# Kernel tuning notes

Measured on AMD Instinct MI355X. Metric: run time of the kernel, lower is better.

The kernel has to match this reference:

```python
import jax, jax.numpy as jnp
import numpy as np

IMAGE_SIZE = 512.0
CENTER_VARIANCE = 0.1
SIZE_VARIANCE = 0.2
NMS_THRESHOLD = 0.45
MAX_CANDIDATES = 400
MAX_PER_IMAGE = 100


def setup_inputs() -> dict:
    key = jax.random.key(0)
    k1, k2, k3, k4 = jax.random.split(key, 4)
    B, P, C = 16, 32768, 81
    cls_logits = jax.random.normal(k1, (B, P, C), dtype=jnp.float32)
    bbox_pred = jax.random.normal(k2, (B, P, 4), dtype=jnp.float32)
    # priors in center form [cx, cy, w, h], normalized coords
    centers = jax.random.uniform(k3, (P, 2), dtype=jnp.float32)
    sizes = jax.random.uniform(k4, (P, 2), dtype=jnp.float32, minval=0.02, maxval=0.4)
    priors = jnp.concatenate([centers, sizes], axis=-1)
    return {"cls_logits": cls_logits, "bbox_pred": bbox_pred, "priors": priors}


def _decode_boxes(locations, priors):
    # locations_to_boxes + center_to_corner_form
    cxy = locations[..., :2] * CENTER_VARIANCE * priors[..., 2:] + priors[..., :2]
    wh = jnp.exp(locations[..., 2:] * SIZE_VARIANCE) * priors[..., 2:]
    return jnp.concatenate([cxy - wh * 0.5, cxy + wh * 0.5], axis=-1)  # [P, 4] xyxy


def _pairwise_iou(boxes):
    # boxes: [N, 4] xyxy
    lt = jnp.maximum(boxes[:, None, :2], boxes[None, :, :2])
    rb = jnp.minimum(boxes[:, None, 2:], boxes[None, :, 2:])
    wh = jnp.clip(rb - lt, 0.0)
    inter = wh[..., 0] * wh[..., 1]
    area = (boxes[:, 2] - boxes[:, 0]) * (boxes[:, 3] - boxes[:, 1])
    union = area[:, None] + area[None, :] - inter
    return inter / jnp.maximum(union, 1e-12)


def _batched_nms_keep(boxes, scores, labels, iou_threshold):
    # boxes sorted by descending score; class-offset trick then greedy NMS
    max_coord = jnp.max(boxes)
    offset = labels.astype(boxes.dtype) * (max_coord + 1.0)
    ious = _pairwise_iou(boxes + offset[:, None])  # [N, N]
    n = boxes.shape[0]
    order = jnp.arange(n)

    def body(i, keep):
        suppress = keep[i] & (ious[i] > iou_threshold) & (order > i)
        return keep & ~suppress

    return jax.lax.fori_loop(0, n, body, jnp.ones((n,), dtype=bool))


def _per_image(logits, locations, priors):
    # logits: [P, C], locations: [P, 4], priors: [P, 4]
    num_classes = logits.shape[-1]
    cm1 = num_classes - 1  # foreground classes (background col 0 dropped)
    scores_all = jax.nn.log_softmax(logits, axis=-1)[:, 1:].reshape(-1)  # [P*(C-1)]
    boxes = _decode_boxes(locations, priors)  # [P, 4]
    # sort_keep_top_k: argsort descending, take top max_candidates
    top_scores, flat_idx = jax.lax.top_k(scores_all, MAX_CANDIDATES)
    box_idx = flat_idx // cm1
    labels = flat_idx % cm1 + 1
    top_boxes = boxes[box_idx] * IMAGE_SIZE  # width == height == image_size
    keep = _batched_nms_keep(top_boxes, top_scores, labels, NMS_THRESHOLD)
    # torch keep[:max_per_image]: first MAX_PER_IMAGE kept entries in score order.
    # Entries are already score-sorted, so top_k on masked scores recovers them.
    masked = jnp.where(keep, top_scores, -jnp.inf)
    _, kidx = jax.lax.top_k(masked, MAX_PER_IMAGE)
    out_scores = jnp.where(keep[kidx], top_scores[kidx], -jnp.inf)  # -inf marks padding
    return top_boxes[kidx], labels[kidx], out_scores


def reference(cls_logits, bbox_pred, priors):
    boxes, labels, scores = jax.vmap(_per_image, in_axes=(0, 0, None))(
        cls_logits, bbox_pred, priors
    )
    return boxes, labels, scores
```

## Files before the change

kernel.cpp:

```cpp
#include <hip/hip_runtime.h>
#include <math.h>

#define BATCH 16
#define P 32768
#define C 81
#define CM1 80
#define NCAND 400
#define NOUT 100
#define NBINS 256
#define SMIN_F (-3.0f)
#define BIN_SCALE (NBINS / 3.0f)
#define SORTN 1024
#define ROWCAP 1024
#define IMG_SZ 512.0f
#define NMS_THR 0.45f
#define NWORDS 7
#define NPAD 448
#define RPB 64

#define OFF_HIST 0
#define OFF_MAXSC 16384
#define NEED_WS (OFF_MAXSC + (size_t)BATCH * P * 4)

__device__ __forceinline__ int score_bin(float sc) {
    int b = (int)((sc - SMIN_F) * BIN_SCALE);
    return b < 0 ? 0 : (b > NBINS - 1 ? NBINS - 1 : b);
}

__device__ __forceinline__ void quad_stats(const float* __restrict__ rowp, int q,
                                           float r[21], float& m, float& l, float& fg) {
#pragma unroll
    for (int k = 0; k < 21; ++k) {
        int c = 4 * k + q;
        r[k] = (c < C) ? rowp[c] : -INFINITY;
    }
    float mm = -INFINITY;
#pragma unroll
    for (int k = 0; k < 21; ++k) mm = fmaxf(mm, r[k]);
    mm = fmaxf(mm, __shfl_xor(mm, 1));
    mm = fmaxf(mm, __shfl_xor(mm, 2));
    float s = 0.0f;
#pragma unroll
    for (int k = 0; k < 21; ++k) {
        int c = 4 * k + q;
        if (c < C) s += __expf(r[k] - mm);
    }
    s += __shfl_xor(s, 1);
    s += __shfl_xor(s, 2);
    float fgm = -INFINITY;
#pragma unroll
    for (int k = 0; k < 21; ++k) {
        int c = 4 * k + q;
        if (c >= 1 && c < C) fgm = fmaxf(fgm, r[k]);
    }
    fgm = fmaxf(fgm, __shfl_xor(fgm, 1));
    fgm = fmaxf(fgm, __shfl_xor(fgm, 2));
    m = mm;
    l = __logf(s);
    fg = fgm;
}

__device__ __forceinline__ unsigned long long pack_key(float v, unsigned id) {
    unsigned bits = __float_as_uint(v);
    unsigned u = (bits & 0x80000000u) ? ~bits : (bits | 0x80000000u);
    return ((unsigned long long)(~u) << 32) | id;
}

__global__ __launch_bounds__(256) void k_hist(const float* __restrict__ logits,
                                              unsigned* __restrict__ hist,
                                              float* __restrict__ maxsc) {
    __shared__ float tile[RPB * C];
    __shared__ unsigned lh[NBINS];
    int img = blockIdx.y;
    int row0 = blockIdx.x * RPB;
    lh[threadIdx.x] = 0;
    const float4* g4 = (const float4*)(logits + ((size_t)img * P + row0) * C);
    float4* t4 = (float4*)tile;
#pragma unroll
    for (int i = 0; i < 6; ++i) {
        int idx = threadIdx.x + i * 256;
        if (idx < RPB * C / 4) t4[idx] = g4[idx];
    }
    __syncthreads();
    int quad = threadIdx.x >> 2, q = threadIdx.x & 3;
    const float* rowp = tile + quad * C;
    float r[21], m, l, fg;
    quad_stats(rowp, q, r, m, l, fg);
    if (q == 0) maxsc[(size_t)img * P + row0 + quad] = (fg - m) - l;
#pragma unroll
    for (int k = 0; k < 21; ++k) {
        int c = 4 * k + q;
        if (c >= 1 && c < C) {
            float sc = (r[k] - m) - l;
            if (sc > SMIN_F) atomicAdd(&lh[score_bin(sc)], 1u);
        }
    }
    __syncthreads();
    unsigned h = lh[threadIdx.x];
    if (h) atomicAdd(&hist[(size_t)img * NBINS + threadIdx.x], h);
}

__global__ __launch_bounds__(1024) void k_post(const float* __restrict__ logits,
                                               const float* __restrict__ bbox,
                                               const float* __restrict__ priors,
                                               const unsigned* __restrict__ hist,
                                               const float* __restrict__ maxsc,
                                               float* __restrict__ out) {
    __shared__ int tb_sh, nrows_sh, ncand_sh;
    __shared__ int rowlist[ROWCAP];
    __shared__ unsigned long long key[SORTN];
    __shared__ float x1[NCAND], y1[NCAND], x2[NCAND], y2[NCAND];
    __shared__ float ox1[NPAD], oy1[NPAD], ox2[NPAD], oy2[NPAD], areas[NPAD];
    __shared__ float scs[NCAND];
    __shared__ int lab[NCAND];
    __shared__ unsigned long long M[NPAD][NWORDS];
    __shared__ unsigned long long keepw_s[NWORDS];
    __shared__ int wpre_s[NWORDS + 1];
    __shared__ float wred[16];
    __shared__ float maxc_sh;
    __shared__ int kidx[NOUT];

    int img = blockIdx.x;
    int tid = threadIdx.x;
    int lane = tid & 63;
    int wv = tid >> 6;

    if (tid == 0) { tb_sh = 0; nrows_sh = 0; ncand_sh = 0; }

    float4 msv[P / 4 / 1024];
    const float4* ms4 = (const float4*)(maxsc + (size_t)img * P);
#pragma unroll
    for (int i = 0; i < P / 4 / 1024; ++i) msv[i] = ms4[tid + i * 1024];

    key[tid] = pack_key(-INFINITY, 0x7FFFFFFFu);

    if (wv == 0) {
        uint4 h4 = ((const uint4*)(hist + (size_t)img * NBINS))[lane];
        unsigned own = h4.x + h4.y + h4.z + h4.w;
        unsigned acc = own;
#pragma unroll
        for (int off = 1; off < 64; off <<= 1) {
            unsigned t = __shfl_down(acc, off);
            if (lane + off < 64) acc += t;
        }
        unsigned above = acc - own;
        unsigned s3 = above + h4.w;
        unsigned s2 = s3 + h4.z;
        unsigned s1 = s2 + h4.y;
        unsigned s0 = s1 + h4.x;
        int best = -1;
        if (s0 >= NCAND) best = 4 * lane + 0;
        if (s1 >= NCAND) best = 4 * lane + 1;
        if (s2 >= NCAND) best = 4 * lane + 2;
        if (s3 >= NCAND) best = 4 * lane + 3;
#pragma unroll
        for (int off = 32; off >= 1; off >>= 1) {
            int o = __shfl_xor(best, off);
            best = best > o ? best : o;
        }
        if (lane == 0) tb_sh = best < 0 ? 0 : best;
    }
    __syncthreads();
    int tb = tb_sh;

#pragma unroll
    for (int i = 0; i < P / 4 / 1024; ++i) {
        float4 v4 = msv[i];
        int rbase = (tid + i * 1024) * 4;
        float vv[4] = {v4.x, v4.y, v4.z, v4.w};
#pragma unroll
        for (int j = 0; j < 4; ++j) {
            if (vv[j] > SMIN_F && score_bin(vv[j]) >= tb) {
                int pos = atomicAdd(&nrows_sh, 1);
                if (pos < ROWCAP) rowlist[pos] = rbase + j;
            }
        }
    }
    __syncthreads();
    int nrows = nrows_sh;
    if (nrows > ROWCAP) nrows = ROWCAP;

    {
        int quad = tid >> 2, q = tid & 3;
        for (int base = 0; base < nrows; base += 256) {
            int ri = base + quad;
            if (ri < nrows) {
                int row = rowlist[ri];
                const float* rowp = logits + ((size_t)img * P + row) * C;
                float r[21], m, l, fg;
                quad_stats(rowp, q, r, m, l, fg);
#pragma unroll
                for (int k = 0; k < 21; ++k) {
                    int c = 4 * k + q;
                    if (c >= 1 && c < C) {
                        float sc = (r[k] - m) - l;
                        if (sc > SMIN_F && score_bin(sc) >= tb) {
                            int pos = atomicAdd(&ncand_sh, 1);
                            if (pos < SORTN)
                                key[pos] = pack_key(sc, (unsigned)(row * CM1 + c - 1));
                        }
                    }
                }
            }
        }
    }
    __syncthreads();

    unsigned long long kr = key[tid];
#pragma unroll
    for (int k2 = 2; k2 <= 64; k2 <<= 1) {
        for (int j = k2 >> 1; j > 0; j >>= 1) {
            unsigned long long pv = __shfl_xor(kr, j);
            bool takeMin = (((tid & j) == 0) == ((tid & k2) == 0));
            bool sel = takeMin ? (pv < kr) : (pv > kr);
            if (sel) kr = pv;
        }
    }
    for (int k2 = 128; k2 <= SORTN; k2 <<= 1) {
        for (int j = k2 >> 1; j >= 64; j >>= 1) {
            __syncthreads();
            key[tid] = kr;
            __syncthreads();
            unsigned long long pv = key[tid ^ j];
            bool takeMin = (((tid & j) == 0) == ((tid & k2) == 0));
            bool sel = takeMin ? (pv < kr) : (pv > kr);
            if (sel) kr = pv;
        }
#pragma unroll
        for (int j = 32; j > 0; j >>= 1) {
            unsigned long long pv = __shfl_xor(kr, j);
            bool takeMin = (((tid & j) == 0) == ((tid & k2) == 0));
            bool sel = takeMin ? (pv < kr) : (pv > kr);
            if (sel) kr = pv;
        }
    }

    if (tid < NCAND) {
        unsigned uu = ~(unsigned)(kr >> 32);
        unsigned bits = (uu & 0x80000000u) ? (uu & 0x7FFFFFFFu) : ~uu;
        scs[tid] = __uint_as_float(bits);
        unsigned f = (unsigned)(kr & 0xFFFFFFFFu);
        if (f > (unsigned)(P * CM1 - 1)) f = (unsigned)(P * CM1 - 1);
        int p = (int)(f / CM1);
        int c = (int)(f % CM1) + 1;
        const float* lp = bbox + ((size_t)img * P + p) * 4;
        const float* pp = priors + (size_t)p * 4;
        float cx = lp[0] * 0.1f * pp[2] + pp[0];
        float cy = lp[1] * 0.1f * pp[3] + pp[1];
        float w = expf(lp[2] * 0.2f) * pp[2];
        float h = expf(lp[3] * 0.2f) * pp[3];
        x1[tid] = (cx - w * 0.5f) * IMG_SZ;
        y1[tid] = (cy - h * 0.5f) * IMG_SZ;
        x2[tid] = (cx + w * 0.5f) * IMG_SZ;
        y2[tid] = (cy + h * 0.5f) * IMG_SZ;
        lab[tid] = c;
    }
    __syncthreads();

    float mx = -INFINITY;
    if (tid < NCAND) mx = fmaxf(fmaxf(x1[tid], y1[tid]), fmaxf(x2[tid], y2[tid]));
#pragma unroll
    for (int off = 32; off >= 1; off >>= 1) mx = fmaxf(mx, __shfl_xor(mx, off));
    if (lane == 0) wred[wv] = mx;
    __syncthreads();
    if (tid == 0) {
        float mm = -INFINITY;
        for (int t = 0; t < 16; ++t) mm = fmaxf(mm, wred[t]);
        maxc_sh = mm;
    }
    __syncthreads();

    if (tid < NPAD) {
        if (tid < NCAND) {
            float off = (float)lab[tid] * (maxc_sh + 1.0f);
            ox1[tid] = x1[tid] + off;
            oy1[tid] = y1[tid] + off;
            ox2[tid] = x2[tid] + off;
            oy2[tid] = y2[tid] + off;
            areas[tid] = (ox2[tid] - ox1[tid]) * (oy2[tid] - oy1[tid]);
        } else {
            ox1[tid] = 1e30f; oy1[tid] = 1e30f;
            ox2[tid] = 1e30f; oy2[tid] = 1e30f;
            areas[tid] = 0.0f;
        }
    }
    __syncthreads();

    for (int i = wv; i < NCAND; i += 16) {
        float a1 = ox1[i], b1 = oy1[i], a2 = ox2[i], b2 = oy2[i], ar = areas[i];
#pragma unroll
        for (int wd = 0; wd < NWORDS; ++wd) {
            int j = wd * 64 + lane;
            float iw_ = fmaxf(fminf(a2, ox2[j]) - fmaxf(a1, ox1[j]), 0.0f);
            float ih_ = fmaxf(fminf(b2, oy2[j]) - fmaxf(b1, oy1[j]), 0.0f);
            float inter = iw_ * ih_;
            float uni = ar + areas[j] - inter;
            float iou = inter / fmaxf(uni, 1e-12f);
            unsigned long long bits = __ballot(iou > NMS_THR);
            if (lane == 0) M[i][wd] = bits;
        }
    }
    __syncthreads();

    if (wv == 0) {
        unsigned long long acc[NWORDS] = {0, 0, 0, 0, 0, 0, 0};
        unsigned long long keepw[NWORDS];
#pragma unroll
        for (int iw = 0; iw < NWORDS; ++iw) {
            unsigned long long mrow[NWORDS];
#pragma unroll
            for (int w = iw; w < NWORDS; ++w) mrow[w] = M[iw * 64 + lane][w];
            unsigned long long sup = acc[iw];
            unsigned long long K = 0;
            int nb = (iw == NWORDS - 1) ? (NCAND - 64 * (NWORDS - 1)) : 64;
            for (int ib = 0; ib < nb; ++ib) {
                if (!((sup >> ib) & 1ull)) {
                    K |= (1ull << ib);
                    int lo, hi;
                    lo = __builtin_amdgcn_readlane((int)(unsigned)mrow[iw], ib);
                    hi = __builtin_amdgcn_readlane((int)(unsigned)(mrow[iw] >> 32), ib);
                    sup |= ((unsigned long long)(unsigned)hi << 32) | (unsigned)lo;
#pragma unroll
                    for (int w = iw + 1; w < NWORDS; ++w) {
                        lo = __builtin_amdgcn_readlane((int)(unsigned)mrow[w], ib);
                        hi = __builtin_amdgcn_readlane((int)(unsigned)(mrow[w] >> 32), ib);
                        acc[w] |= ((unsigned long long)(unsigned)hi << 32) | (unsigned)lo;
                    }
                }
            }
            keepw[iw] = K;
        }
        if (lane == 0) {
            int a = 0;
#pragma unroll
            for (int w = 0; w < NWORDS; ++w) {
                keepw_s[w] = keepw[w];
                wpre_s[w] = a;
                a += __popcll(keepw[w]);
            }
            wpre_s[NWORDS] = a;
        }
    }
    __syncthreads();

    if (tid < NCAND) {
        int w = tid >> 6, bb = tid & 63;
        unsigned long long kwv = keepw_s[w];
        bool kp = (kwv >> bb) & 1ull;
        unsigned long long below_mask = (bb == 0) ? 0ull : (~0ull >> (64 - bb));
        int below = wpre_s[w] + __popcll(kwv & below_mask);
        int nkept = wpre_s[NWORDS];
        int pos = kp ? below : nkept + (tid - below);
        if (pos < NOUT) kidx[pos] = tid;
    }
    __syncthreads();

    if (tid < NOUT) {
        int i = kidx[tid];
        bool kp = (keepw_s[i >> 6] >> (i & 63)) & 1ull;
        float* ob = out + ((size_t)img * NOUT + tid) * 4;
        ob[0] = x1[i];
        ob[1] = y1[i];
        ob[2] = x2[i];
        ob[3] = y2[i];
        out[(size_t)BATCH * NOUT * 4 + (size_t)img * NOUT + tid] = (float)lab[i];
        out[(size_t)BATCH * NOUT * 4 + (size_t)BATCH * NOUT + (size_t)img * NOUT + tid] =
            kp ? scs[i] : -INFINITY;
    }
}

extern "C" void kernel_launch(void* const* d_in, const int* in_sizes, int n_in,
                              void* d_out, int out_size, void* d_ws, size_t ws_size,
                              hipStream_t stream) {
    const float* logits = (const float*)d_in[0];
    const float* bbox = (const float*)d_in[1];
    const float* priors = (const float*)d_in[2];
    float* out = (float*)d_out;
    char* ws = (char*)d_ws;

    unsigned* hist = (unsigned*)(ws + OFF_HIST);
    float* maxsc = (float*)(ws + OFF_MAXSC);

    hipMemsetAsync(ws, 0, OFF_MAXSC, stream);

    dim3 g1(P / RPB, BATCH);
    k_hist<<<g1, 256, 0, stream>>>(logits, hist, maxsc);
    k_post<<<BATCH, 1024, 0, stream>>>(logits, bbox, priors, hist, maxsc, out);
}
```

Baseline: 339.6 us.

## Emit candidate keys from histogram pass instead of recomputing rows in post kernel

```diff
diff --git a/kernel.cpp b/kernel.cpp
--- a/kernel.cpp
+++ b/kernel.cpp
@@ -11,16 +11,18 @@
 #define SMIN_F (-3.0f)
 #define BIN_SCALE (NBINS / 3.0f)
 #define SORTN 1024
-#define ROWCAP 1024
 #define IMG_SZ 512.0f
 #define NMS_THR 0.45f
 #define NWORDS 7
 #define NPAD 448
 #define RPB 64
+#define LCAP 2048
+#define CAND_CAP 131072
 
 #define OFF_HIST 0
-#define OFF_MAXSC 16384
-#define NEED_WS (OFF_MAXSC + (size_t)BATCH * P * 4)
+#define OFF_GCNT 16384
+#define OFF_CAND 16448
+#define NEED_WS (OFF_CAND + (size_t)BATCH * CAND_CAP * 8)
 
 __device__ __forceinline__ int score_bin(float sc) {
     int b = (int)((sc - SMIN_F) * BIN_SCALE);
@@ -66,14 +68,25 @@
     return ((unsigned long long)(~u) << 32) | id;
 }
 
+__device__ __forceinline__ float unpack_score(unsigned long long kk) {
+    unsigned uu = ~(unsigned)(kk >> 32);
+    unsigned bits = (uu & 0x80000000u) ? (uu & 0x7FFFFFFFu) : ~uu;
+    return __uint_as_float(bits);
+}
+
 __global__ __launch_bounds__(256) void k_hist(const float* __restrict__ logits,
                                               unsigned* __restrict__ hist,
-                                              float* __restrict__ maxsc) {
+                                              unsigned* __restrict__ gcnt,
+                                              unsigned long long* __restrict__ cand) {
     __shared__ float tile[RPB * C];
     __shared__ unsigned lh[NBINS];
+    __shared__ unsigned long long lc[LCAP];
+    __shared__ int lcnt_sh;
+    __shared__ int base_sh;
     int img = blockIdx.y;
     int row0 = blockIdx.x * RPB;
     lh[threadIdx.x] = 0;
+    if (threadIdx.x == 0) lcnt_sh = 0;
     const float4* g4 = (const float4*)(logits + ((size_t)img * P + row0) * C);
     float4* t4 = (float4*)tile;
 #pragma unroll
@@ -86,28 +99,42 @@
     const float* rowp = tile + quad * C;
     float r[21], m, l, fg;
     quad_stats(rowp, q, r, m, l, fg);
-    if (q == 0) maxsc[(size_t)img * P + row0 + quad] = (fg - m) - l;
+    (void)fg;
+    int row = row0 + quad;
 #pragma unroll
     for (int k = 0; k < 21; ++k) {
         int c = 4 * k + q;
         if (c >= 1 && c < C) {
             float sc = (r[k] - m) - l;
-            if (sc > SMIN_F) atomicAdd(&lh[score_bin(sc)], 1u);
+            if (sc > SMIN_F) {
+                atomicAdd(&lh[score_bin(sc)], 1u);
+                int pos = atomicAdd(&lcnt_sh, 1);
+                if (pos < LCAP) lc[pos] = pack_key(sc, (unsigned)(row * CM1 + c - 1));
+            }
         }
     }
     __syncthreads();
     unsigned h = lh[threadIdx.x];
     if (h) atomicAdd(&hist[(size_t)img * NBINS + threadIdx.x], h);
-}
-
-__global__ __launch_bounds__(1024) void k_post(const float* __restrict__ logits,
-                                               const float* __restrict__ bbox,
+    int n = lcnt_sh;
+    if (n > LCAP) n = LCAP;
+    if (threadIdx.x == 0) base_sh = (int)atomicAdd(&gcnt[img], (unsigned)n);
+    __syncthreads();
+    int base = base_sh;
+    unsigned long long* dst = cand + (size_t)img * CAND_CAP;
+    for (int i = threadIdx.x; i < n; i += 256) {
+        int pos = base + i;
+        if (pos < CAND_CAP) dst[pos] = lc[i];
+    }
+}
+
+__global__ __launch_bounds__(1024) void k_post(const float* __restrict__ bbox,
                                                const float* __restrict__ priors,
                                                const unsigned* __restrict__ hist,
-                                               const float* __restrict__ maxsc,
+                                               const unsigned* __restrict__ gcnt,
+                                               const unsigned long long* __restrict__ cand,
                                                float* __restrict__ out) {
-    __shared__ int tb_sh, nrows_sh, ncand_sh;
-    __shared__ int rowlist[ROWCAP];
+    __shared__ int tb_sh, ncand_sh;
     __shared__ unsigned long long key[SORTN];
     __shared__ float x1[NCAND], y1[NCAND], x2[NCAND], y2[NCAND];
     __shared__ float ox1[NPAD], oy1[NPAD], ox2[NPAD], oy2[NPAD], areas[NPAD];
@@ -125,13 +152,7 @@
     int lane = tid & 63;
     int wv = tid >> 6;
 
-    if (tid == 0) { tb_sh = 0; nrows_sh = 0; ncand_sh = 0; }
-
-    float4 msv[P / 4 / 1024];
-    const float4* ms4 = (const float4*)(maxsc + (size_t)img * P);
-#pragma unroll
-    for (int i = 0; i < P / 4 / 1024; ++i) msv[i] = ms4[tid + i * 1024];
-
+    if (tid == 0) { tb_sh = 0; ncand_sh = 0; }
     key[tid] = pack_key(-INFINITY, 0x7FFFFFFFu);
 
     if (wv == 0) {
@@ -163,44 +184,15 @@
     __syncthreads();
     int tb = tb_sh;
 
-#pragma unroll
-    for (int i = 0; i < P / 4 / 1024; ++i) {
-        float4 v4 = msv[i];
-        int rbase = (tid + i * 1024) * 4;
-        float vv[4] = {v4.x, v4.y, v4.z, v4.w};
-#pragma unroll
-        for (int j = 0; j < 4; ++j) {
-            if (vv[j] > SMIN_F && score_bin(vv[j]) >= tb) {
-                int pos = atomicAdd(&nrows_sh, 1);
-                if (pos < ROWCAP) rowlist[pos] = rbase + j;
-            }
-        }
-    }
-    __syncthreads();
-    int nrows = nrows_sh;
-    if (nrows > ROWCAP) nrows = ROWCAP;
-
     {
-        int quad = tid >> 2, q = tid & 3;
-        for (int base = 0; base < nrows; base += 256) {
-            int ri = base + quad;
-            if (ri < nrows) {
-                int row = rowlist[ri];
-                const float* rowp = logits + ((size_t)img * P + row) * C;
-                float r[21], m, l, fg;
-                quad_stats(rowp, q, r, m, l, fg);
-#pragma unroll
-                for (int k = 0; k < 21; ++k) {
-                    int c = 4 * k + q;
-                    if (c >= 1 && c < C) {
-                        float sc = (r[k] - m) - l;
-                        if (sc > SMIN_F && score_bin(sc) >= tb) {
-                            int pos = atomicAdd(&ncand_sh, 1);
-                            if (pos < SORTN)
-                                key[pos] = pack_key(sc, (unsigned)(row * CM1 + c - 1));
-                        }
-                    }
-                }
+        int n = (int)gcnt[img];
+        if (n > CAND_CAP) n = CAND_CAP;
+        const unsigned long long* src = cand + (size_t)img * CAND_CAP;
+        for (int i = tid; i < n; i += 1024) {
+            unsigned long long kk = src[i];
+            if (score_bin(unpack_score(kk)) >= tb) {
+                int pos = atomicAdd(&ncand_sh, 1);
+                if (pos < SORTN) key[pos] = kk;
             }
         }
     }
@@ -236,9 +228,7 @@
     }
 
     if (tid < NCAND) {
-        unsigned uu = ~(unsigned)(kr >> 32);
-        unsigned bits = (uu & 0x80000000u) ? (uu & 0x7FFFFFFFu) : ~uu;
-        scs[tid] = __uint_as_float(bits);
+        scs[tid] = unpack_score(kr);
         unsigned f = (unsigned)(kr & 0xFFFFFFFFu);
         if (f > (unsigned)(P * CM1 - 1)) f = (unsigned)(P * CM1 - 1);
         int p = (int)(f / CM1);
@@ -379,11 +369,12 @@
     char* ws = (char*)d_ws;
 
     unsigned* hist = (unsigned*)(ws + OFF_HIST);
-    float* maxsc = (float*)(ws + OFF_MAXSC);
-
-    hipMemsetAsync(ws, 0, OFF_MAXSC, stream);
+    unsigned* gcnt = (unsigned*)(ws + OFF_GCNT);
+    unsigned long long* cand = (unsigned long long*)(ws + OFF_CAND);
+
+    hipMemsetAsync(ws, 0, OFF_CAND, stream);
 
     dim3 g1(P / RPB, BATCH);
-    k_hist<<<g1, 256, 0, stream>>>(logits, hist, maxsc);
-    k_post<<<BATCH, 1024, 0, stream>>>(logits, bbox, priors, hist, maxsc, out);
-}
+    k_hist<<<g1, 256, 0, stream>>>(logits, hist, gcnt, cand);
+    k_post<<<BATCH, 1024, 0, stream>>>(bbox, priors, hist, gcnt, cand, out);
+}
```

Measured after the change: 392.9 us. 15.7% more time.
